# Performance work log

Measured on AMD Instinct MI355X. Metric: run time of the kernel, lower is better.

## Reference

```python
import jax, jax.numpy as jnp
import numpy as np

N, E, H, L, G = 50000, 500000, 128, 4, 1000
EPS = 1e-7      # GENConv message eps
LN_EPS = 1e-5   # torch LayerNorm default


def setup_inputs() -> dict:
    key = jax.random.key(0)
    ks = jax.random.split(key, 24)
    d = {}
    d["x"] = jax.random.normal(ks[0], (N, 9), jnp.float32)
    d["edge_index"] = jax.random.randint(ks[1], (2, E), 0, N, jnp.int32)
    d["edge_attr"] = jax.random.normal(ks[2], (E, 3), jnp.float32)
    d["batch"] = jnp.sort(jax.random.randint(ks[3], (N,), 0, G, jnp.int32))
    s9, s3, sh, s2h = 1/np.sqrt(9), 1/np.sqrt(3), 1/np.sqrt(H), 1/np.sqrt(2*H)
    u = lambda k, shp, s: jax.random.uniform(k, shp, jnp.float32, -s, s)
    d["enc_node_W"] = u(ks[4], (9, H), s9)
    d["enc_node_b"] = u(ks[5], (H,), s9)
    d["enc_edge_W"] = u(ks[6], (3, H), s3)
    d["enc_edge_b"] = u(ks[7], (H,), s3)
    d["ln_g"] = jnp.ones((L, H), jnp.float32)   # DeepGCNLayer pre-norm affine
    d["ln_b"] = jnp.zeros((L, H), jnp.float32)
    d["W1"] = u(ks[8], (L, H, 2*H), sh)          # GENConv MLP layer 1
    d["b1"] = u(ks[9], (L, 2*H), sh)
    d["mlp_ln_g"] = jnp.ones((L, 2*H), jnp.float32)
    d["mlp_ln_b"] = jnp.zeros((L, 2*H), jnp.float32)
    d["W2"] = u(ks[10], (L, 2*H, H), s2h)        # GENConv MLP layer 2
    d["b2"] = u(ks[11], (L, H), s2h)
    d["t"] = jnp.ones((L,), jnp.float32)         # learnable softmax temperature, init 1.0
    return d


def layernorm(x, g, b):
    mu = x.mean(-1, keepdims=True)
    var = ((x - mu) ** 2).mean(-1, keepdims=True)
    return (x - mu) / jnp.sqrt(var + LN_EPS) * g + b


def genconv(h, src, dst, ea, t, W1, b1, lg, lb, W2, b2):
    # message: relu(x_j + edge_attr) + eps   -> [E, H]
    msg = jax.nn.relu(h[src] + ea) + EPS
    # softmax aggregation over incoming edges, per channel
    logits = t * msg
    m = jax.ops.segment_max(logits, dst, num_segments=N)
    num = jnp.exp(logits - m[dst])
    den = jax.ops.segment_sum(num, dst, num_segments=N)
    alpha = num / den[dst]
    agg = jax.ops.segment_sum(msg * alpha, dst, num_segments=N)
    out = agg + h  # root residual inside GENConv
    z = jax.nn.relu(layernorm(out @ W1 + b1, lg, lb))
    return z @ W2 + b2


def reference(x, edge_index, edge_attr, batch, enc_node_W, enc_node_b,
              enc_edge_W, enc_edge_b, ln_g, ln_b, W1, b1, mlp_ln_g, mlp_ln_b,
              W2, b2, t):
    src, dst = edge_index[0], edge_index[1]
    h = x @ enc_node_W + enc_node_b            # node encoder  [N, H]
    ea = edge_attr @ enc_edge_W + enc_edge_b   # edge encoder  [E, H]
    # layer 0: conv only (DeeperGCN forward uses layers[0].conv directly)
    h = genconv(h, src, dst, ea, t[0], W1[0], b1[0], mlp_ln_g[0], mlp_ln_b[0], W2[0], b2[0])
    # layers 1..L-1: res+ block: x + conv(relu(LN(x))); dropout is identity (eval)
    for i in range(1, L):
        z = jax.nn.relu(layernorm(h, ln_g[i], ln_b[i]))
        h = h + genconv(z, src, dst, ea, t[i], W1[i], b1[i], mlp_ln_g[i], mlp_ln_b[i], W2[i], b2[i])
    h = jax.nn.relu(layernorm(h, ln_g[0], ln_b[0]))  # reuses layer-0 norm
    # global mean pool over graphs
    counts = jax.ops.segment_sum(jnp.ones((N,), h.dtype), batch, num_segments=G)
    sums = jax.ops.segment_sum(h, batch, num_segments=G)
    return sums / jnp.maximum(counts, 1.0)[:, None]
```

## Files before the change

kernel.cpp:

```cpp
#include <hip/hip_runtime.h>

#define NN 50000
#define NE 500000
#define HD 128
#define HD2 256
#define NL 4
#define NG 1000

constexpr float MSG_EPS = 1e-7f;
constexpr float LNEPS   = 1e-5f;

typedef float  f32x4  __attribute__((ext_vector_type(4)));
typedef __bf16 bf16x8 __attribute__((ext_vector_type(8)));

__device__ __forceinline__ unsigned short f2b(float f) {
    unsigned int u = __float_as_uint(f);
    unsigned int r = u + 0x7FFFu + ((u >> 16) & 1u);
    return (unsigned short)(r >> 16);
}
__device__ __forceinline__ float b2f(unsigned short h) {
    return __uint_as_float(((unsigned int)h) << 16);
}

__global__ void k_encode_nodes(const float* __restrict__ x, const float* __restrict__ W,
                               const float* __restrict__ b, unsigned short* __restrict__ zb) {
    int n = blockIdx.x;
    int c = threadIdx.x;
    float xr[9];
#pragma unroll
    for (int k = 0; k < 9; k++) xr[k] = x[n * 9 + k];
    float acc = b[c];
#pragma unroll
    for (int k = 0; k < 9; k++) acc = fmaf(xr[k], W[k * HD + c], acc);
    zb[n * HD + c] = f2b(acc);
}

__global__ void k_prep(const float* __restrict__ W1, const float* __restrict__ W2,
                       unsigned short* __restrict__ W1T, unsigned short* __restrict__ W2T) {
    int idx = blockIdx.x * 256 + threadIdx.x;
    {
        int k = idx & 127, n = (idx >> 7) & 255, l = idx >> 15;
        W1T[idx] = f2b(W1[(l * 128 + k) * 256 + n]);
    }
    {
        int k = idx & 255, n = (idx >> 8) & 127, l = idx >> 15;
        W2T[idx] = f2b(W2[(l * 256 + k) * 128 + n]);
    }
}

__global__ void k_hist(const int* __restrict__ dst, int* __restrict__ counts) {
    int e = blockIdx.x * blockDim.x + threadIdx.x;
    if (e < NE) atomicAdd(&counts[dst[e]], 1);
}

#define SCAN_B 512
__global__ void k_scan1(const int* __restrict__ counts, int* __restrict__ incl,
                        int* __restrict__ bsum) {
    __shared__ int s[SCAN_B];
    int i = blockIdx.x * SCAN_B + threadIdx.x;
    int v = (i < NN) ? counts[i] : 0;
    s[threadIdx.x] = v;
    __syncthreads();
    for (int off = 1; off < SCAN_B; off <<= 1) {
        int t = (threadIdx.x >= off) ? s[threadIdx.x - off] : 0;
        __syncthreads();
        s[threadIdx.x] += t;
        __syncthreads();
    }
    if (i < NN) incl[i] = s[threadIdx.x];
    if (threadIdx.x == SCAN_B - 1) bsum[blockIdx.x] = s[threadIdx.x];
}

__global__ void k_scan2(const int* __restrict__ bsum, int* __restrict__ boff, int nb) {
    __shared__ int s[128];
    int v = (threadIdx.x < nb) ? bsum[threadIdx.x] : 0;
    s[threadIdx.x] = v;
    __syncthreads();
    for (int off = 1; off < 128; off <<= 1) {
        int t = (threadIdx.x >= off) ? s[threadIdx.x - off] : 0;
        __syncthreads();
        s[threadIdx.x] += t;
        __syncthreads();
    }
    if (threadIdx.x < nb) boff[threadIdx.x] = s[threadIdx.x] - v;
}

__global__ void k_scan3(const int* __restrict__ incl, const int* __restrict__ boff,
                        int* __restrict__ row_start) {
    int i = blockIdx.x * SCAN_B + threadIdx.x;
    if (i < NN) row_start[i + 1] = incl[i] + boff[blockIdx.x];
    if (i == 0) row_start[0] = 0;
}

__global__ void k_scatter(const int* __restrict__ src, const int* __restrict__ dst,
                          const float* __restrict__ eattr, const int* __restrict__ row_start,
                          int* __restrict__ cursor, float4* __restrict__ aperm) {
    int e = blockIdx.x * blockDim.x + threadIdx.x;
    if (e >= NE) return;
    int d = dst[e];
    int p = row_start[d] + atomicAdd(&cursor[d], 1);
    float4 v;
    v.x = eattr[e * 3 + 0];
    v.y = eattr[e * 3 + 1];
    v.z = eattr[e * 3 + 2];
    v.w = __int_as_float(src[e]);
    aperm[p] = v;
}

__global__ __launch_bounds__(256) void k_aggregate(const unsigned short* __restrict__ zb,
                                                   const float4* __restrict__ aperm,
                                                   const int* __restrict__ row_start,
                                                   const float* __restrict__ We,
                                                   const float* __restrict__ be,
                                                   const float* __restrict__ t, int layer,
                                                   unsigned int* __restrict__ outb) {
    int w = threadIdx.x >> 6, lane = threadIdx.x & 63;
    int n = blockIdx.x * 4 + w;
    if (n >= NN) return;
    int c = lane * 2;
    float2 w0 = *(const float2*)&We[c];
    float2 w1 = *(const float2*)&We[HD + c];
    float2 w2 = *(const float2*)&We[2 * HD + c];
    float2 bb = *(const float2*)&be[c];
    float tv = t[layer];
    int s0 = row_start[n], s1 = row_start[n + 1];
    float num0 = 0.f, num1 = 0.f, wm0 = 0.f, wm1 = 0.f;
    const unsigned int* z32 = (const unsigned int*)zb;
    int p = s0;
    for (; p + 2 <= s1; p += 2) {
        float4 a0 = aperm[p];
        float4 a1 = aperm[p + 1];
        int sj0 = __float_as_int(a0.w);
        int sj1 = __float_as_int(a1.w);
        unsigned int za = z32[sj0 * 64 + lane];
        unsigned int zc = z32[sj1 * 64 + lane];
        float zax = b2f((unsigned short)za), zay = b2f((unsigned short)(za >> 16));
        float zcx = b2f((unsigned short)zc), zcy = b2f((unsigned short)(zc >> 16));
        float ea0x = fmaf(a0.x, w0.x, fmaf(a0.y, w1.x, fmaf(a0.z, w2.x, bb.x)));
        float ea0y = fmaf(a0.x, w0.y, fmaf(a0.y, w1.y, fmaf(a0.z, w2.y, bb.y)));
        float ea1x = fmaf(a1.x, w0.x, fmaf(a1.y, w1.x, fmaf(a1.z, w2.x, bb.x)));
        float ea1y = fmaf(a1.x, w0.y, fmaf(a1.y, w1.y, fmaf(a1.z, w2.y, bb.y)));
        float m0x = fmaxf(zax + ea0x, 0.f) + MSG_EPS;
        float m0y = fmaxf(zay + ea0y, 0.f) + MSG_EPS;
        float m1x = fmaxf(zcx + ea1x, 0.f) + MSG_EPS;
        float m1y = fmaxf(zcy + ea1y, 0.f) + MSG_EPS;
        float e0x = __expf(tv * m0x), e0y = __expf(tv * m0y);
        float e1x = __expf(tv * m1x), e1y = __expf(tv * m1y);
        num0 += e0x + e1x;
        num1 += e0y + e1y;
        wm0 = fmaf(m0x, e0x, fmaf(m1x, e1x, wm0));
        wm1 = fmaf(m0y, e0y, fmaf(m1y, e1y, wm1));
    }
    if (p < s1) {
        float4 a = aperm[p];
        int sj = __float_as_int(a.w);
        unsigned int za = z32[sj * 64 + lane];
        float zax = b2f((unsigned short)za), zay = b2f((unsigned short)(za >> 16));
        float eax = fmaf(a.x, w0.x, fmaf(a.y, w1.x, fmaf(a.z, w2.x, bb.x)));
        float eay = fmaf(a.x, w0.y, fmaf(a.y, w1.y, fmaf(a.z, w2.y, bb.y)));
        float mx = fmaxf(zax + eax, 0.f) + MSG_EPS;
        float my = fmaxf(zay + eay, 0.f) + MSG_EPS;
        float ex = __expf(tv * mx), ey = __expf(tv * my);
        num0 += ex;
        num1 += ey;
        wm0 = fmaf(mx, ex, wm0);
        wm1 = fmaf(my, ey, wm1);
    }
    unsigned int zn = z32[n * 64 + lane];
    float ox = ((s1 > s0) ? (wm0 / num0) : 0.f) + b2f((unsigned short)zn);
    float oy = ((s1 > s0) ? (wm1 / num1) : 0.f) + b2f((unsigned short)(zn >> 16));
    outb[n * 64 + lane] = (unsigned int)f2b(ox) | ((unsigned int)f2b(oy) << 16);
}

#define BM 32
#define HS_LD 264

__global__ __launch_bounds__(256) void k_mlp(const unsigned short* __restrict__ outb,
                                             const unsigned short* __restrict__ W1T,
                                             const float* __restrict__ b1l,
                                             const float* __restrict__ lgl,
                                             const float* __restrict__ lbl,
                                             const unsigned short* __restrict__ W2T,
                                             const float* __restrict__ b2l,
                                             float* __restrict__ h,
                                             const float* __restrict__ gn,
                                             const float* __restrict__ bn,
                                             unsigned short* __restrict__ zb,
                                             int add_residual) {
    __shared__ __align__(16) unsigned short Hs[BM * HS_LD];

    int nb = blockIdx.x * BM;
    int tid = threadIdx.x;
    int w = tid >> 6, lane = tid & 63, q = lane >> 4, i = lane & 15;

    f32x4 acc[2][4];
#pragma unroll
    for (int rt = 0; rt < 2; rt++)
#pragma unroll
        for (int ct = 0; ct < 4; ct++) acc[rt][ct] = (f32x4){0.f, 0.f, 0.f, 0.f};

#pragma unroll
    for (int ks = 0; ks < 4; ks++) {
        bf16x8 af[2], bf[4];
#pragma unroll
        for (int rt = 0; rt < 2; rt++) {
            int row = nb + rt * 16 + i;
            if (row < NN)
                af[rt] = *(const bf16x8*)&outb[(size_t)row * HD + ks * 32 + q * 8];
            else
                af[rt] = (bf16x8)(__bf16)0.f;
        }
#pragma unroll
        for (int ct = 0; ct < 4; ct++)
            bf[ct] = *(const bf16x8*)&W1T[(w * 64 + ct * 16 + i) * HD + ks * 32 + q * 8];
#pragma unroll
        for (int rt = 0; rt < 2; rt++)
#pragma unroll
            for (int ct = 0; ct < 4; ct++)
                acc[rt][ct] = __builtin_amdgcn_mfma_f32_16x16x32_bf16(af[rt], bf[ct],
                                                                     acc[rt][ct], 0, 0, 0);
    }

    float b1c[4];
#pragma unroll
    for (int ct = 0; ct < 4; ct++) b1c[ct] = b1l[w * 64 + ct * 16 + i];
#pragma unroll
    for (int rt = 0; rt < 2; rt++)
#pragma unroll
        for (int ct = 0; ct < 4; ct++)
#pragma unroll
            for (int r = 0; r < 4; r++)
                Hs[(rt * 16 + q * 4 + r) * HS_LD + w * 64 + ct * 16 + i] =
                    f2b(acc[rt][ct][r] + b1c[ct]);
    __syncthreads();

    {
        float4 g4 = *(const float4*)&lgl[lane * 4];
        float4 be4 = *(const float4*)&lbl[lane * 4];
        for (int r = 0; r < 8; r++) {
            int row = w * 8 + r;
            ushort4 hv = *(ushort4*)&Hs[row * HS_LD + lane * 4];
            float v0 = b2f(hv.x), v1 = b2f(hv.y), v2 = b2f(hv.z), v3 = b2f(hv.w);
            float s = v0 + v1 + v2 + v3;
            float sq = v0 * v0 + v1 * v1 + v2 * v2 + v3 * v3;
#pragma unroll
            for (int m = 32; m >= 1; m >>= 1) {
                s += __shfl_xor(s, m);
                sq += __shfl_xor(sq, m);
            }
            float mu = s * (1.f / 256.f);
            float var = sq * (1.f / 256.f) - mu * mu;
            float inv = rsqrtf(var + LNEPS);
            ushort4 o;
            o.x = f2b(fmaxf(fmaf((v0 - mu) * inv, g4.x, be4.x), 0.f));
            o.y = f2b(fmaxf(fmaf((v1 - mu) * inv, g4.y, be4.y), 0.f));
            o.z = f2b(fmaxf(fmaf((v2 - mu) * inv, g4.z, be4.z), 0.f));
            o.w = f2b(fmaxf(fmaf((v3 - mu) * inv, g4.w, be4.w), 0.f));
            *(ushort4*)&Hs[row * HS_LD + lane * 4] = o;
        }
    }
    __syncthreads();

    f32x4 acc2[2][2];
#pragma unroll
    for (int rt = 0; rt < 2; rt++)
#pragma unroll
        for (int ct = 0; ct < 2; ct++) acc2[rt][ct] = (f32x4){0.f, 0.f, 0.f, 0.f};

#pragma unroll
    for (int ks = 0; ks < 8; ks++) {
        bf16x8 af[2], bf[2];
#pragma unroll
        for (int rt = 0; rt < 2; rt++)
            af[rt] = *(const bf16x8*)&Hs[(rt * 16 + i) * HS_LD + ks * 32 + q * 8];
#pragma unroll
        for (int ct = 0; ct < 2; ct++)
            bf[ct] = *(const bf16x8*)&W2T[(w * 32 + ct * 16 + i) * HD2 + ks * 32 + q * 8];
#pragma unroll
        for (int rt = 0; rt < 2; rt++)
#pragma unroll
            for (int ct = 0; ct < 2; ct++)
                acc2[rt][ct] = __builtin_amdgcn_mfma_f32_16x16x32_bf16(af[rt], bf[ct],
                                                                      acc2[rt][ct], 0, 0, 0);
    }
    __syncthreads();

    float* Hsf = (float*)Hs;
    float b2c[2];
#pragma unroll
    for (int ct = 0; ct < 2; ct++) b2c[ct] = b2l[w * 32 + ct * 16 + i];
#pragma unroll
    for (int rt = 0; rt < 2; rt++)
#pragma unroll
        for (int ct = 0; ct < 2; ct++)
#pragma unroll
            for (int r = 0; r < 4; r++) {
                int rloc = rt * 16 + q * 4 + r;
                int row = nb + rloc;
                int col = w * 32 + ct * 16 + i;
                if (row < NN) {
                    size_t idx = (size_t)row * HD + col;
                    float v = acc2[rt][ct][r] + b2c[ct];
                    float hn = add_residual ? (h[idx] + v) : v;
                    h[idx] = hn;
                    Hsf[rloc * 132 + col] = hn;
                }
            }
    __syncthreads();

    {
        float2 gg = *(const float2*)&gn[lane * 2];
        float2 cc = *(const float2*)&bn[lane * 2];
        for (int rr = 0; rr < 8; rr++) {
            int rloc = w * 8 + rr;
            int row = nb + rloc;
            if (row >= NN) break;
            float2 v = *(float2*)&Hsf[rloc * 132 + lane * 2];
            float s = v.x + v.y, sq = v.x * v.x + v.y * v.y;
#pragma unroll
            for (int m = 32; m >= 1; m >>= 1) {
                s += __shfl_xor(s, m);
                sq += __shfl_xor(sq, m);
            }
            float mu = s * (1.f / 128.f);
            float var = sq * (1.f / 128.f) - mu * mu;
            float inv = rsqrtf(var + LNEPS);
            float z0 = fmaxf(fmaf((v.x - mu) * inv, gg.x, cc.x), 0.f);
            float z1 = fmaxf(fmaf((v.y - mu) * inv, gg.y, cc.y), 0.f);
            ((unsigned int*)zb)[(size_t)row * 64 + lane] =
                (unsigned int)f2b(z0) | ((unsigned int)f2b(z1) << 16);
        }
    }
}

__global__ void k_gbounds(const int* __restrict__ batch, int* __restrict__ gstart) {
    int g = blockIdx.x * blockDim.x + threadIdx.x;
    if (g > NG) return;
    int lo = 0, hi = NN;
    while (lo < hi) {
        int mid = (lo + hi) >> 1;
        if (batch[mid] < g) lo = mid + 1;
        else hi = mid;
    }
    gstart[g] = lo;
}

__global__ void k_pool(const unsigned short* __restrict__ zb, const int* __restrict__ gstart,
                       float* __restrict__ out) {
    int g = blockIdx.x;
    int c = threadIdx.x;
    int a = gstart[g], b = gstart[g + 1];
    float s0 = 0.f, s1 = 0.f;
    int n = a;
    for (; n + 2 <= b; n += 2) {
        s0 += b2f(zb[(size_t)n * HD + c]);
        s1 += b2f(zb[(size_t)(n + 1) * HD + c]);
    }
    if (n < b) s0 += b2f(zb[(size_t)n * HD + c]);
    out[g * HD + c] = (s0 + s1) / fmaxf((float)(b - a), 1.f);
}

extern "C" void kernel_launch(void* const* d_in, const int* in_sizes, int n_in, void* d_out,
                              int out_size, void* d_ws, size_t ws_size, hipStream_t stream) {
    const float* x     = (const float*)d_in[0];
    const int* ei      = (const int*)d_in[1];
    const float* eattr = (const float*)d_in[2];
    const int* batch   = (const int*)d_in[3];
    const float* encW  = (const float*)d_in[4];
    const float* encB  = (const float*)d_in[5];
    const float* eW    = (const float*)d_in[6];
    const float* eB    = (const float*)d_in[7];
    const float* ln_g  = (const float*)d_in[8];
    const float* ln_b  = (const float*)d_in[9];
    const float* W1    = (const float*)d_in[10];
    const float* b1    = (const float*)d_in[11];
    const float* mlg   = (const float*)d_in[12];
    const float* mlb   = (const float*)d_in[13];
    const float* W2    = (const float*)d_in[14];
    const float* b2    = (const float*)d_in[15];
    const float* t     = (const float*)d_in[16];
    const int* src = ei;
    const int* dst = ei + NE;

    char* w = (char*)d_ws;
    auto alloc = [&](size_t bytes) {
        char* p = w;
        w += (bytes + 255) & ~size_t(255);
        return p;
    };
    float* h             = (float*)alloc(sizeof(float) * NN * HD);
    unsigned short* zb   = (unsigned short*)alloc(sizeof(unsigned short) * NN * HD);
    unsigned int* outb   = (unsigned int*)alloc(sizeof(unsigned int) * NN * HD / 2);
    float4* aperm        = (float4*)alloc(sizeof(float4) * NE);
    int* row_start       = (int*)alloc(sizeof(int) * (NN + 1));
    int* counts          = (int*)alloc(sizeof(int) * NN);
    int* cursor          = (int*)alloc(sizeof(int) * NN);
    int* incl            = (int*)alloc(sizeof(int) * NN);
    int* bsum            = (int*)alloc(sizeof(int) * 128);
    int* boff            = (int*)alloc(sizeof(int) * 128);
    int* gstart          = (int*)alloc(sizeof(int) * (NG + 1));
    unsigned short* W1T  = (unsigned short*)alloc(sizeof(unsigned short) * NL * HD * HD2);
    unsigned short* W2T  = (unsigned short*)alloc(sizeof(unsigned short) * NL * HD2 * HD);

    hipMemsetAsync(counts, 0, sizeof(int) * NN, stream);
    hipMemsetAsync(cursor, 0, sizeof(int) * NN, stream);

    k_prep<<<512, 256, 0, stream>>>(W1, W2, W1T, W2T);
    k_encode_nodes<<<NN, HD, 0, stream>>>(x, encW, encB, zb);
    k_hist<<<(NE + 255) / 256, 256, 0, stream>>>(dst, counts);
    int nsb = (NN + SCAN_B - 1) / SCAN_B;
    k_scan1<<<nsb, SCAN_B, 0, stream>>>(counts, incl, bsum);
    k_scan2<<<1, 128, 0, stream>>>(bsum, boff, nsb);
    k_scan3<<<nsb, SCAN_B, 0, stream>>>(incl, boff, row_start);
    k_scatter<<<(NE + 255) / 256, 256, 0, stream>>>(src, dst, eattr, row_start, cursor, aperm);
    k_gbounds<<<(NG + 256) / 256, 256, 0, stream>>>(batch, gstart);

    for (int l = 0; l < NL; l++) {
        k_aggregate<<<(NN + 3) / 4, 256, 0, stream>>>(zb, aperm, row_start, eW, eB, t, l, outb);
        int ln_next = (l + 1) % NL;
        k_mlp<<<(NN + BM - 1) / BM, 256, 0, stream>>>(
            (const unsigned short*)outb, W1T + (size_t)l * HD * HD2, b1 + l * HD2,
            mlg + l * HD2, mlb + l * HD2, W2T + (size_t)l * HD2 * HD, b2 + l * HD, h,
            ln_g + ln_next * HD, ln_b + ln_next * HD, zb, l > 0);
    }
    k_pool<<<NG, HD, 0, stream>>>(zb, gstart, (float*)d_out);
}
```

Baseline: 558.8 us.

## Restructure aggregate per half-row and fuse LayerNorm stats into MLP register epilogues

The aggregate kernel now gives each node two wavefronts, one channel per lane, with 4-edge unrolling. Each lane issues 16-bit gathers instead of 32-bit ones. The MLP kernel double-buffers its MFMA operand loads. It computes both LayerNorm statistics from accumulator registers using shuffles plus a small shared-memory cross-wave reduction, which removes the separate shared-memory LN passes. The residual stream h is stored in bf16 instead of fp32 to halve its traffic, at the cost of accumulated precision loss across layers.

```diff
diff --git a/kernel.cpp b/kernel.cpp
--- a/kernel.cpp
+++ b/kernel.cpp
@@ -107,69 +107,50 @@
     aperm[p] = v;
 }
 
-__global__ __launch_bounds__(256) void k_aggregate(const unsigned short* __restrict__ zb,
+__device__ __forceinline__ void edge_acc1(float4 a, float z, float w0, float w1, float w2,
+                                          float bb, float tv, float& num, float& wm) {
+    float ea = fmaf(a.x, w0, fmaf(a.y, w1, fmaf(a.z, w2, bb)));
+    float m = fmaxf(z + ea, 0.f) + MSG_EPS;
+    float e = __expf(tv * m);
+    num += e;
+    wm = fmaf(m, e, wm);
+}
+
+__global__ __launch_bounds__(256) void k_aggregate(const unsigned short* __restrict__ zbin,
                                                    const float4* __restrict__ aperm,
                                                    const int* __restrict__ row_start,
                                                    const float* __restrict__ We,
                                                    const float* __restrict__ be,
                                                    const float* __restrict__ t, int layer,
-                                                   unsigned int* __restrict__ outb) {
+                                                   unsigned short* __restrict__ outb) {
     int w = threadIdx.x >> 6, lane = threadIdx.x & 63;
-    int n = blockIdx.x * 4 + w;
+    int n = blockIdx.x * 2 + (w >> 1);
     if (n >= NN) return;
-    int c = lane * 2;
-    float2 w0 = *(const float2*)&We[c];
-    float2 w1 = *(const float2*)&We[HD + c];
-    float2 w2 = *(const float2*)&We[2 * HD + c];
-    float2 bb = *(const float2*)&be[c];
+    int c = ((w & 1) << 6) | lane;
+    float w0 = We[c], w1 = We[HD + c], w2 = We[2 * HD + c], bb = be[c];
     float tv = t[layer];
     int s0 = row_start[n], s1 = row_start[n + 1];
-    float num0 = 0.f, num1 = 0.f, wm0 = 0.f, wm1 = 0.f;
-    const unsigned int* z32 = (const unsigned int*)zb;
+    float num = 0.f, wm = 0.f;
     int p = s0;
-    for (; p + 2 <= s1; p += 2) {
-        float4 a0 = aperm[p];
-        float4 a1 = aperm[p + 1];
-        int sj0 = __float_as_int(a0.w);
-        int sj1 = __float_as_int(a1.w);
-        unsigned int za = z32[sj0 * 64 + lane];
-        unsigned int zc = z32[sj1 * 64 + lane];
-        float zax = b2f((unsigned short)za), zay = b2f((unsigned short)(za >> 16));
-        float zcx = b2f((unsigned short)zc), zcy = b2f((unsigned short)(zc >> 16));
-        float ea0x = fmaf(a0.x, w0.x, fmaf(a0.y, w1.x, fmaf(a0.z, w2.x, bb.x)));
-        float ea0y = fmaf(a0.x, w0.y, fmaf(a0.y, w1.y, fmaf(a0.z, w2.y, bb.y)));
-        float ea1x = fmaf(a1.x, w0.x, fmaf(a1.y, w1.x, fmaf(a1.z, w2.x, bb.x)));
-        float ea1y = fmaf(a1.x, w0.y, fmaf(a1.y, w1.y, fmaf(a1.z, w2.y, bb.y)));
-        float m0x = fmaxf(zax + ea0x, 0.f) + MSG_EPS;
-        float m0y = fmaxf(zay + ea0y, 0.f) + MSG_EPS;
-        float m1x = fmaxf(zcx + ea1x, 0.f) + MSG_EPS;
-        float m1y = fmaxf(zcy + ea1y, 0.f) + MSG_EPS;
-        float e0x = __expf(tv * m0x), e0y = __expf(tv * m0y);
-        float e1x = __expf(tv * m1x), e1y = __expf(tv * m1y);
-        num0 += e0x + e1x;
-        num1 += e0y + e1y;
-        wm0 = fmaf(m0x, e0x, fmaf(m1x, e1x, wm0));
-        wm1 = fmaf(m0y, e0y, fmaf(m1y, e1y, wm1));
-    }
-    if (p < s1) {
+    for (; p + 4 <= s1; p += 4) {
+        float4 a0 = aperm[p], a1 = aperm[p + 1], a2 = aperm[p + 2], a3 = aperm[p + 3];
+        float z0 = b2f(zbin[(size_t)__float_as_int(a0.w) * HD + c]);
+        float z1 = b2f(zbin[(size_t)__float_as_int(a1.w) * HD + c]);
+        float z2 = b2f(zbin[(size_t)__float_as_int(a2.w) * HD + c]);
+        float z3 = b2f(zbin[(size_t)__float_as_int(a3.w) * HD + c]);
+        edge_acc1(a0, z0, w0, w1, w2, bb, tv, num, wm);
+        edge_acc1(a1, z1, w0, w1, w2, bb, tv, num, wm);
+        edge_acc1(a2, z2, w0, w1, w2, bb, tv, num, wm);
+        edge_acc1(a3, z3, w0, w1, w2, bb, tv, num, wm);
+    }
+    for (; p < s1; p++) {
         float4 a = aperm[p];
-        int sj = __float_as_int(a.w);
-        unsigned int za = z32[sj * 64 + lane];
-        float zax = b2f((unsigned short)za), zay = b2f((unsigned short)(za >> 16));
-        float eax = fmaf(a.x, w0.x, fmaf(a.y, w1.x, fmaf(a.z, w2.x, bb.x)));
-        float eay = fmaf(a.x, w0.y, fmaf(a.y, w1.y, fmaf(a.z, w2.y, bb.y)));
-        float mx = fmaxf(zax + eax, 0.f) + MSG_EPS;
-        float my = fmaxf(zay + eay, 0.f) + MSG_EPS;
-        float ex = __expf(tv * mx), ey = __expf(tv * my);
-        num0 += ex;
-        num1 += ey;
-        wm0 = fmaf(mx, ex, wm0);
-        wm1 = fmaf(my, ey, wm1);
-    }
-    unsigned int zn = z32[n * 64 + lane];
-    float ox = ((s1 > s0) ? (wm0 / num0) : 0.f) + b2f((unsigned short)zn);
-    float oy = ((s1 > s0) ? (wm1 / num1) : 0.f) + b2f((unsigned short)(zn >> 16));
-    outb[n * 64 + lane] = (unsigned int)f2b(ox) | ((unsigned int)f2b(oy) << 16);
+        float z = b2f(zbin[(size_t)__float_as_int(a.w) * HD + c]);
+        edge_acc1(a, z, w0, w1, w2, bb, tv, num, wm);
+    }
+    float zn = b2f(zbin[(size_t)n * HD + c]);
+    float o = ((s1 > s0) ? (wm / num) : 0.f) + zn;
+    outb[(size_t)n * HD + c] = f2b(o);
 }
 
 #define BM 32
@@ -182,12 +163,14 @@
                                              const float* __restrict__ lbl,
                                              const unsigned short* __restrict__ W2T,
                                              const float* __restrict__ b2l,
-                                             float* __restrict__ h,
+                                             unsigned short* __restrict__ h,
                                              const float* __restrict__ gn,
                                              const float* __restrict__ bn,
                                              unsigned short* __restrict__ zb,
                                              int add_residual) {
     __shared__ __align__(16) unsigned short Hs[BM * HS_LD];
+    __shared__ __align__(16) float2 st1[2][16][4];
+    __shared__ __align__(16) float2 st2[2][16][4];
 
     int nb = blockIdx.x * BM;
     int tid = threadIdx.x;
@@ -199,137 +182,238 @@
 #pragma unroll
         for (int ct = 0; ct < 4; ct++) acc[rt][ct] = (f32x4){0.f, 0.f, 0.f, 0.f};
 
+    bf16x8 acur[2], bcur[4];
+#pragma unroll
+    for (int rt = 0; rt < 2; rt++) {
+        int row = nb + rt * 16 + i;
+        acur[rt] = (row < NN) ? *(const bf16x8*)&outb[(size_t)row * HD + q * 8]
+                              : (bf16x8)(__bf16)0.f;
+    }
+#pragma unroll
+    for (int ct = 0; ct < 4; ct++)
+        bcur[ct] = *(const bf16x8*)&W1T[(w * 64 + ct * 16 + i) * HD + q * 8];
+
 #pragma unroll
     for (int ks = 0; ks < 4; ks++) {
-        bf16x8 af[2], bf[4];
-#pragma unroll
-        for (int rt = 0; rt < 2; rt++) {
-            int row = nb + rt * 16 + i;
-            if (row < NN)
-                af[rt] = *(const bf16x8*)&outb[(size_t)row * HD + ks * 32 + q * 8];
-            else
-                af[rt] = (bf16x8)(__bf16)0.f;
-        }
-#pragma unroll
-        for (int ct = 0; ct < 4; ct++)
-            bf[ct] = *(const bf16x8*)&W1T[(w * 64 + ct * 16 + i) * HD + ks * 32 + q * 8];
-#pragma unroll
-        for (int rt = 0; rt < 2; rt++)
+        bf16x8 anxt[2], bnxt[4];
+        if (ks < 3) {
+#pragma unroll
+            for (int rt = 0; rt < 2; rt++) {
+                int row = nb + rt * 16 + i;
+                anxt[rt] = (row < NN)
+                               ? *(const bf16x8*)&outb[(size_t)row * HD + (ks + 1) * 32 + q * 8]
+                               : (bf16x8)(__bf16)0.f;
+            }
 #pragma unroll
             for (int ct = 0; ct < 4; ct++)
-                acc[rt][ct] = __builtin_amdgcn_mfma_f32_16x16x32_bf16(af[rt], bf[ct],
-                                                                     acc[rt][ct], 0, 0, 0);
-    }
-
-    float b1c[4];
-#pragma unroll
-    for (int ct = 0; ct < 4; ct++) b1c[ct] = b1l[w * 64 + ct * 16 + i];
+                bnxt[ct] =
+                    *(const bf16x8*)&W1T[(w * 64 + ct * 16 + i) * HD + (ks + 1) * 32 + q * 8];
+        }
+#pragma unroll
+        for (int rt = 0; rt < 2; rt++)
+#pragma unroll
+            for (int ct = 0; ct < 4; ct++)
+                acc[rt][ct] =
+                    __builtin_amdgcn_mfma_f32_16x16x32_bf16(acur[rt], bcur[ct], acc[rt][ct],
+                                                            0, 0, 0);
+        if (ks < 3) {
+#pragma unroll
+            for (int rt = 0; rt < 2; rt++) acur[rt] = anxt[rt];
+#pragma unroll
+            for (int ct = 0; ct < 4; ct++) bcur[ct] = bnxt[ct];
+        }
+    }
+
+#pragma unroll
+    for (int ct = 0; ct < 4; ct++) {
+        float bb = b1l[w * 64 + ct * 16 + i];
+#pragma unroll
+        for (int rt = 0; rt < 2; rt++)
+#pragma unroll
+            for (int r = 0; r < 4; r++) acc[rt][ct][r] += bb;
+    }
+
+    {
+        float sv[2][4], qv[2][4];
+#pragma unroll
+        for (int rt = 0; rt < 2; rt++)
+#pragma unroll
+            for (int r = 0; r < 4; r++) {
+                float s = acc[rt][0][r] + acc[rt][1][r] + acc[rt][2][r] + acc[rt][3][r];
+                float sq = 0.f;
+#pragma unroll
+                for (int ct = 0; ct < 4; ct++) sq = fmaf(acc[rt][ct][r], acc[rt][ct][r], sq);
+                sv[rt][r] = s;
+                qv[rt][r] = sq;
+            }
+#pragma unroll
+        for (int m = 1; m <= 8; m <<= 1)
+#pragma unroll
+            for (int rt = 0; rt < 2; rt++)
+#pragma unroll
+                for (int r = 0; r < 4; r++) {
+                    sv[rt][r] += __shfl_xor(sv[rt][r], m);
+                    qv[rt][r] += __shfl_xor(qv[rt][r], m);
+                }
+        if (i == 0) {
+#pragma unroll
+            for (int rt = 0; rt < 2; rt++)
+#pragma unroll
+                for (int r = 0; r < 4; r++)
+                    st1[rt][q * 4 + r][w] = make_float2(sv[rt][r], qv[rt][r]);
+        }
+    }
+    __syncthreads();
+
+    {
+        float mu[2][4], inv[2][4];
+#pragma unroll
+        for (int rt = 0; rt < 2; rt++)
+#pragma unroll
+            for (int r = 0; r < 4; r++) {
+                const float4* sp = (const float4*)&st1[rt][q * 4 + r][0];
+                float4 a = sp[0], b = sp[1];
+                float S = a.x + a.z + b.x + b.z;
+                float Q = a.y + a.w + b.y + b.w;
+                float m_ = S * (1.f / 256.f);
+                float v_ = Q * (1.f / 256.f) - m_ * m_;
+                mu[rt][r] = m_;
+                inv[rt][r] = rsqrtf(v_ + LNEPS);
+            }
+#pragma unroll
+        for (int ct = 0; ct < 4; ct++) {
+            float g = lgl[w * 64 + ct * 16 + i];
+            float c = lbl[w * 64 + ct * 16 + i];
+#pragma unroll
+            for (int rt = 0; rt < 2; rt++)
+#pragma unroll
+                for (int r = 0; r < 4; r++) {
+                    float v =
+                        fmaxf(fmaf((acc[rt][ct][r] - mu[rt][r]) * inv[rt][r], g, c), 0.f);
+                    Hs[(rt * 16 + q * 4 + r) * HS_LD + w * 64 + ct * 16 + i] = f2b(v);
+                }
+        }
+    }
+    __syncthreads();
+
+    unsigned short hold[2][2][4] = {};
+    if (add_residual) {
+#pragma unroll
+        for (int rt = 0; rt < 2; rt++)
+#pragma unroll
+            for (int ct = 0; ct < 2; ct++)
+#pragma unroll
+                for (int r = 0; r < 4; r++) {
+                    int row = nb + rt * 16 + q * 4 + r;
+                    hold[rt][ct][r] =
+                        (row < NN) ? h[(size_t)row * HD + w * 32 + ct * 16 + i] : 0;
+                }
+    }
+
+    f32x4 acc2[2][2];
 #pragma unroll
     for (int rt = 0; rt < 2; rt++)
 #pragma unroll
-        for (int ct = 0; ct < 4; ct++)
-#pragma unroll
-            for (int r = 0; r < 4; r++)
-                Hs[(rt * 16 + q * 4 + r) * HS_LD + w * 64 + ct * 16 + i] =
-                    f2b(acc[rt][ct][r] + b1c[ct]);
+        for (int ct = 0; ct < 2; ct++) acc2[rt][ct] = (f32x4){0.f, 0.f, 0.f, 0.f};
+
+    bf16x8 hc[2], bc[2];
+#pragma unroll
+    for (int rt = 0; rt < 2; rt++) hc[rt] = *(const bf16x8*)&Hs[(rt * 16 + i) * HS_LD + q * 8];
+#pragma unroll
+    for (int ct = 0; ct < 2; ct++)
+        bc[ct] = *(const bf16x8*)&W2T[(w * 32 + ct * 16 + i) * HD2 + q * 8];
+
+#pragma unroll
+    for (int ks = 0; ks < 8; ks++) {
+        bf16x8 hn[2], bn2[2];
+        if (ks < 7) {
+#pragma unroll
+            for (int rt = 0; rt < 2; rt++)
+                hn[rt] = *(const bf16x8*)&Hs[(rt * 16 + i) * HS_LD + (ks + 1) * 32 + q * 8];
+#pragma unroll
+            for (int ct = 0; ct < 2; ct++)
+                bn2[ct] =
+                    *(const bf16x8*)&W2T[(w * 32 + ct * 16 + i) * HD2 + (ks + 1) * 32 + q * 8];
+        }
+#pragma unroll
+        for (int rt = 0; rt < 2; rt++)
+#pragma unroll
+            for (int ct = 0; ct < 2; ct++)
+                acc2[rt][ct] = __builtin_amdgcn_mfma_f32_16x16x32_bf16(hc[rt], bc[ct],
+                                                                      acc2[rt][ct], 0, 0, 0);
+        if (ks < 7) {
+#pragma unroll
+            for (int rt = 0; rt < 2; rt++) hc[rt] = hn[rt];
+#pragma unroll
+            for (int ct = 0; ct < 2; ct++) bc[ct] = bn2[ct];
+        }
+    }
+
+#pragma unroll
+    for (int ct = 0; ct < 2; ct++) {
+        float bb = b2l[w * 32 + ct * 16 + i];
+#pragma unroll
+        for (int rt = 0; rt < 2; rt++)
+#pragma unroll
+            for (int r = 0; r < 4; r++) {
+                float v = acc2[rt][ct][r] + bb;
+                if (add_residual) v += b2f(hold[rt][ct][r]);
+                acc2[rt][ct][r] = v;
+                int row = nb + rt * 16 + q * 4 + r;
+                if (row < NN) h[(size_t)row * HD + w * 32 + ct * 16 + i] = f2b(v);
+            }
+    }
+
+    {
+        float sv[2][4], qv[2][4];
+#pragma unroll
+        for (int rt = 0; rt < 2; rt++)
+#pragma unroll
+            for (int r = 0; r < 4; r++) {
+                sv[rt][r] = acc2[rt][0][r] + acc2[rt][1][r];
+                qv[rt][r] = fmaf(acc2[rt][0][r], acc2[rt][0][r],
+                                 acc2[rt][1][r] * acc2[rt][1][r]);
+            }
+#pragma unroll
+        for (int m = 1; m <= 8; m <<= 1)
+#pragma unroll
+            for (int rt = 0; rt < 2; rt++)
+#pragma unroll
+                for (int r = 0; r < 4; r++) {
+                    sv[rt][r] += __shfl_xor(sv[rt][r], m);
+                    qv[rt][r] += __shfl_xor(qv[rt][r], m);
+                }
+        if (i == 0) {
+#pragma unroll
+            for (int rt = 0; rt < 2; rt++)
+#pragma unroll
+                for (int r = 0; r < 4; r++)
+                    st2[rt][q * 4 + r][w] = make_float2(sv[rt][r], qv[rt][r]);
+        }
+    }
     __syncthreads();
 
     {
-        float4 g4 = *(const float4*)&lgl[lane * 4];
-        float4 be4 = *(const float4*)&lbl[lane * 4];
-        for (int r = 0; r < 8; r++) {
-            int row = w * 8 + r;
-            ushort4 hv = *(ushort4*)&Hs[row * HS_LD + lane * 4];
-            float v0 = b2f(hv.x), v1 = b2f(hv.y), v2 = b2f(hv.z), v3 = b2f(hv.w);
-            float s = v0 + v1 + v2 + v3;
-            float sq = v0 * v0 + v1 * v1 + v2 * v2 + v3 * v3;
-#pragma unroll
-            for (int m = 32; m >= 1; m >>= 1) {
-                s += __shfl_xor(s, m);
-                sq += __shfl_xor(sq, m);
-            }
-            float mu = s * (1.f / 256.f);
-            float var = sq * (1.f / 256.f) - mu * mu;
-            float inv = rsqrtf(var + LNEPS);
-            ushort4 o;
-            o.x = f2b(fmaxf(fmaf((v0 - mu) * inv, g4.x, be4.x), 0.f));
-            o.y = f2b(fmaxf(fmaf((v1 - mu) * inv, g4.y, be4.y), 0.f));
-            o.z = f2b(fmaxf(fmaf((v2 - mu) * inv, g4.z, be4.z), 0.f));
-            o.w = f2b(fmaxf(fmaf((v3 - mu) * inv, g4.w, be4.w), 0.f));
-            *(ushort4*)&Hs[row * HS_LD + lane * 4] = o;
-        }
-    }
-    __syncthreads();
-
-    f32x4 acc2[2][2];
-#pragma unroll
-    for (int rt = 0; rt < 2; rt++)
-#pragma unroll
-        for (int ct = 0; ct < 2; ct++) acc2[rt][ct] = (f32x4){0.f, 0.f, 0.f, 0.f};
-
-#pragma unroll
-    for (int ks = 0; ks < 8; ks++) {
-        bf16x8 af[2], bf[2];
-#pragma unroll
-        for (int rt = 0; rt < 2; rt++)
-            af[rt] = *(const bf16x8*)&Hs[(rt * 16 + i) * HS_LD + ks * 32 + q * 8];
-#pragma unroll
-        for (int ct = 0; ct < 2; ct++)
-            bf[ct] = *(const bf16x8*)&W2T[(w * 32 + ct * 16 + i) * HD2 + ks * 32 + q * 8];
-#pragma unroll
-        for (int rt = 0; rt < 2; rt++)
-#pragma unroll
-            for (int ct = 0; ct < 2; ct++)
-                acc2[rt][ct] = __builtin_amdgcn_mfma_f32_16x16x32_bf16(af[rt], bf[ct],
-                                                                      acc2[rt][ct], 0, 0, 0);
-    }
-    __syncthreads();
-
-    float* Hsf = (float*)Hs;
-    float b2c[2];
-#pragma unroll
-    for (int ct = 0; ct < 2; ct++) b2c[ct] = b2l[w * 32 + ct * 16 + i];
-#pragma unroll
-    for (int rt = 0; rt < 2; rt++)
-#pragma unroll
-        for (int ct = 0; ct < 2; ct++)
+#pragma unroll
+        for (int rt = 0; rt < 2; rt++)
 #pragma unroll
             for (int r = 0; r < 4; r++) {
-                int rloc = rt * 16 + q * 4 + r;
-                int row = nb + rloc;
-                int col = w * 32 + ct * 16 + i;
-                if (row < NN) {
-                    size_t idx = (size_t)row * HD + col;
-                    float v = acc2[rt][ct][r] + b2c[ct];
-                    float hn = add_residual ? (h[idx] + v) : v;
-                    h[idx] = hn;
-                    Hsf[rloc * 132 + col] = hn;
+                const float4* sp = (const float4*)&st2[rt][q * 4 + r][0];
+                float4 a = sp[0], b = sp[1];
+                float S = a.x + a.z + b.x + b.z;
+                float Q = a.y + a.w + b.y + b.w;
+                float m_ = S * (1.f / 128.f);
+                float v_ = Q * (1.f / 128.f) - m_ * m_;
+                float iv = rsqrtf(v_ + LNEPS);
+#pragma unroll
+                for (int ct = 0; ct < 2; ct++) {
+                    float g = gn[w * 32 + ct * 16 + i];
+                    float c = bn[w * 32 + ct * 16 + i];
+                    float v = fmaxf(fmaf((acc2[rt][ct][r] - m_) * iv, g, c), 0.f);
+                    int row = nb + rt * 16 + q * 4 + r;
+                    if (row < NN) zb[(size_t)row * HD + w * 32 + ct * 16 + i] = f2b(v);
                 }
             }
-    __syncthreads();
-
-    {
-        float2 gg = *(const float2*)&gn[lane * 2];
-        float2 cc = *(const float2*)&bn[lane * 2];
-        for (int rr = 0; rr < 8; rr++) {
-            int rloc = w * 8 + rr;
-            int row = nb + rloc;
-            if (row >= NN) break;
-            float2 v = *(float2*)&Hsf[rloc * 132 + lane * 2];
-            float s = v.x + v.y, sq = v.x * v.x + v.y * v.y;
-#pragma unroll
-            for (int m = 32; m >= 1; m >>= 1) {
-                s += __shfl_xor(s, m);
-                sq += __shfl_xor(sq, m);
-            }
-            float mu = s * (1.f / 128.f);
-            float var = sq * (1.f / 128.f) - mu * mu;
-            float inv = rsqrtf(var + LNEPS);
-            float z0 = fmaxf(fmaf((v.x - mu) * inv, gg.x, cc.x), 0.f);
-            float z1 = fmaxf(fmaf((v.y - mu) * inv, gg.y, cc.y), 0.f);
-            ((unsigned int*)zb)[(size_t)row * 64 + lane] =
-                (unsigned int)f2b(z0) | ((unsigned int)f2b(z1) << 16);
-        }
     }
 }
 
@@ -388,9 +472,9 @@
         w += (bytes + 255) & ~size_t(255);
         return p;
     };
-    float* h             = (float*)alloc(sizeof(float) * NN * HD);
+    unsigned short* h    = (unsigned short*)alloc(sizeof(unsigned short) * NN * HD);
     unsigned short* zb   = (unsigned short*)alloc(sizeof(unsigned short) * NN * HD);
-    unsigned int* outb   = (unsigned int*)alloc(sizeof(unsigned int) * NN * HD / 2);
+    unsigned short* outb = (unsigned short*)alloc(sizeof(unsigned short) * NN * HD);
     float4* aperm        = (float4*)alloc(sizeof(float4) * NE);
     int* row_start       = (int*)alloc(sizeof(int) * (NN + 1));
     int* counts          = (int*)alloc(sizeof(int) * NN);
@@ -416,12 +500,12 @@
     k_gbounds<<<(NG + 256) / 256, 256, 0, stream>>>(batch, gstart);
 
     for (int l = 0; l < NL; l++) {
-        k_aggregate<<<(NN + 3) / 4, 256, 0, stream>>>(zb, aperm, row_start, eW, eB, t, l, outb);
+        k_aggregate<<<(NN + 1) / 2, 256, 0, stream>>>(zb, aperm, row_start, eW, eB, t, l, outb);
         int ln_next = (l + 1) % NL;
         k_mlp<<<(NN + BM - 1) / BM, 256, 0, stream>>>(
-            (const unsigned short*)outb, W1T + (size_t)l * HD * HD2, b1 + l * HD2,
-            mlg + l * HD2, mlb + l * HD2, W2T + (size_t)l * HD2 * HD, b2 + l * HD, h,
-            ln_g + ln_next * HD, ln_b + ln_next * HD, zb, l > 0);
+            outb, W1T + (size_t)l * HD * HD2, b1 + l * HD2, mlg + l * HD2, mlb + l * HD2,
+            W2T + (size_t)l * HD2 * HD, b2 + l * HD, h, ln_g + ln_next * HD,
+            ln_b + ln_next * HD, zb, l > 0);
     }
     k_pool<<<NG, HD, 0, stream>>>(zb, gstart, (float*)d_out);
 }
```

Result: slower. 596.3 us (+6.7%).
